# Performance work log

Hardware: AMD Instinct MI355X
Metric: run time of the kernel (lower is better)

The kernel has to match this reference:

```python
import jax, jax.numpy as jnp
import numpy as np

EPS = 1e-5


def gcn_conv(x, src, dst, n_nodes, W, b):
    # x: [B, N, Fin]; src/dst: [E+N] (self loops included); W: [Fout, Fin]
    h = jnp.einsum('bnf,of->bno', x, W)                      # [B, N, Fout]
    deg = jnp.zeros((n_nodes,), h.dtype).at[dst].add(1.0)    # in-degree of A+I
    dinv = jnp.where(deg > 0, 1.0 / jnp.sqrt(deg), 0.0)
    norm = dinv[src] * dinv[dst]                             # [E+N]
    msg = h[:, src, :] * norm[None, :, None]                 # gather along node axis
    out = jnp.zeros_like(h).at[:, dst, :].add(msg)           # scatter-add aggregate
    return out + b


def batchnorm_nodes(x, gamma, beta):
    # torch BatchNorm1d(N) on [B, N, C]: channel axis is N, stats over (B, C)
    mean = jnp.mean(x, axis=(0, 2), keepdims=True)
    var = jnp.mean(jnp.square(x - mean), axis=(0, 2), keepdims=True)
    xn = (x - mean) * jax.lax.rsqrt(var + EPS)
    return xn * gamma[None, :, None] + beta[None, :, None]


def setup_inputs() -> dict:
    key = jax.random.key(0)
    ks = jax.random.split(key, 20)
    B, N, FIN, D, OUT, E = 4096, 64, 67, 2048, 2, 512
    s = 0.1
    d = {}
    d['x_fingerprints'] = jax.random.normal(ks[0], (B, D), jnp.float32)
    d['x_node_features'] = jax.random.normal(ks[1], (B, N, FIN), jnp.float32)
    d['edge_list'] = jax.random.randint(ks[2], (2, E), 0, N)
    d['W1'] = jax.random.normal(ks[3], (64, FIN), jnp.float32) * s
    d['b1'] = jax.random.normal(ks[4], (64,), jnp.float32) * s
    d['g1'] = 1.0 + jax.random.normal(ks[5], (N,), jnp.float32) * s
    d['be1'] = jax.random.normal(ks[6], (N,), jnp.float32) * s
    d['W2'] = jax.random.normal(ks[7], (32, 64), jnp.float32) * s
    d['b2'] = jax.random.normal(ks[8], (32,), jnp.float32) * s
    d['g2'] = 1.0 + jax.random.normal(ks[9], (N,), jnp.float32) * s
    d['be2'] = jax.random.normal(ks[10], (N,), jnp.float32) * s
    d['Wl1'] = jax.random.normal(ks[11], (400, D), jnp.float32) * (s / 4)
    d['bl1'] = jax.random.normal(ks[12], (400,), jnp.float32) * s
    d['Wl2'] = jax.random.normal(ks[13], (64, 400), jnp.float32) * s
    d['bl2'] = jax.random.normal(ks[14], (64,), jnp.float32) * s
    d['Wfc'] = jax.random.normal(ks[15], (OUT, 96), jnp.float32) * s
    d['bfc'] = jax.random.normal(ks[16], (OUT,), jnp.float32) * s
    return d


def reference(x_fingerprints, x_node_features, edge_list, W1, b1, g1, be1,
              W2, b2, g2, be2, Wl1, bl1, Wl2, bl2, Wfc, bfc):
    B, N, _ = x_node_features.shape
    loops = jnp.arange(N)
    src = jnp.concatenate([edge_list[0], loops])  # add self loops (GCNConv default)
    dst = jnp.concatenate([edge_list[1], loops])
    g = gcn_conv(x_node_features, src, dst, N, W1, b1)
    g = jax.nn.relu(batchnorm_nodes(g, g1, be1))
    g = gcn_conv(g, src, dst, N, W2, b2)
    g = jax.nn.relu(batchnorm_nodes(g, g2, be2))           # [B, N, 32]
    pooled = jnp.max(g, axis=1)                             # global_max_pool -> [B, 32]
    h = jax.nn.relu(x_fingerprints @ Wl1.T + bl1)
    h = jax.nn.relu(h @ Wl2.T + bl2)                        # [B, 64]
    out = jnp.concatenate([pooled, h], axis=1) @ Wfc.T + bfc
    return out
```

## Files before the change

### kernel.cpp

```cpp
#include <hip/hip_runtime.h>
#include <hip/hip_bf16.h>
#include <math.h>

typedef __bf16 bf16;
typedef __attribute__((ext_vector_type(8))) __bf16 bf16x8;
typedef __attribute__((ext_vector_type(4))) __bf16 bf16x4;
typedef __attribute__((ext_vector_type(4))) float f32x4;

#define EPSBN 1e-5f
#define B_    4096
#define N_    64
#define FIN_  67
#define E_    512
#define TOT_E 576
#define NSLOT 128

__global__ __launch_bounds__(256) void k0_prep(const int* __restrict__ edge,
    float* __restrict__ partials,
    int* __restrict__ g_off, int* __restrict__ g_src, float* __restrict__ g_nrm)
{
    int tid = threadIdx.x;
    for (int i = blockIdx.x * 256 + tid; i < NSLOT * 64 * 4; i += gridDim.x * 256)
        partials[i] = 0.f;
    if (blockIdx.x != 0) return;

    __shared__ int ssrc[TOT_E], sdst[TOT_E];
    __shared__ int deg[N_], cnt[N_], off[N_ + 1];
    __shared__ float dinv[N_];
    for (int i = tid; i < TOT_E; i += 256) {
        int s, d;
        if (i < E_) { s = edge[i]; d = edge[E_ + i]; }
        else        { s = i - E_; d = i - E_; }
        ssrc[i] = s; sdst[i] = d;
    }
    if (tid < N_) { deg[tid] = 0; cnt[tid] = 0; }
    __syncthreads();
    for (int i = tid; i < TOT_E; i += 256) atomicAdd(&deg[sdst[i]], 1);
    __syncthreads();
    if (tid < N_) {
        dinv[tid] = rsqrtf((float)deg[tid]);
        int v = deg[tid];
        for (int o = 1; o < 64; o <<= 1) { int u = __shfl_up(v, o); if (tid >= o) v += u; }
        off[tid] = v - deg[tid];
        if (tid == 63) off[N_] = v;
    }
    __syncthreads();
    for (int i = tid; i < TOT_E; i += 256) {
        int d = sdst[i];
        int p = off[d] + atomicAdd(&cnt[d], 1);
        g_src[p] = ssrc[i];
        g_nrm[p] = dinv[ssrc[i]] * dinv[d];
    }
    if (tid <= N_) g_off[tid] = off[tid];
}

__global__ __launch_bounds__(256) void k1_gcn1(
    const float* __restrict__ x,
    const float* __restrict__ W1,
    const float* __restrict__ b1,
    const int* __restrict__ g_off, const int* __restrict__ g_src,
    const float* __restrict__ g_nrm,
    bf16* __restrict__ g1out,
    float* __restrict__ part1)
{
    __shared__ union {
        struct { bf16 xa[64 * 104]; bf16 wb[64 * 104]; } s0;
        struct { float hs[64 * 68]; } s1;
    } u;
    __shared__ int coff[N_ + 1];
    __shared__ int csrc[TOT_E];
    __shared__ float cnrm[TOT_E];

    int tid = threadIdx.x;
    int b = blockIdx.x;
    for (int i = tid; i <= N_; i += 256) coff[i] = g_off[i];
    for (int i = tid; i < TOT_E; i += 256) { csrc[i] = g_src[i]; cnrm[i] = g_nrm[i]; }

    const float* xb = x + (size_t)b * (N_ * FIN_);
    for (int i = tid; i < N_ * FIN_; i += 256) {
        int n = i / FIN_, f = i % FIN_;
        u.s0.xa[n * 104 + f] = (bf16)xb[i];
    }
    for (int i = tid; i < N_ * FIN_; i += 256) {
        int n = i / FIN_, f = i % FIN_;
        u.s0.wb[n * 104 + f] = (bf16)W1[i];
    }
    for (int i = tid; i < 64 * 29; i += 256) {
        int n = i / 29, f = 67 + i % 29;
        u.s0.xa[n * 104 + f] = (bf16)0.f;
        u.s0.wb[n * 104 + f] = (bf16)0.f;
    }
    __syncthreads();

    int w = tid >> 6, lane = tid & 63, q = lane >> 4, r15 = lane & 15;
    f32x4 z4 = {0.f, 0.f, 0.f, 0.f};
    f32x4 acc[4] = {z4, z4, z4, z4};
    int arow = w * 16 + r15;
#pragma unroll
    for (int kt = 0; kt < 3; ++kt) {
        bf16x8 a = *(const bf16x8*)&u.s0.xa[arow * 104 + kt * 32 + q * 8];
#pragma unroll
        for (int nt = 0; nt < 4; ++nt) {
            bf16x8 bb = *(const bf16x8*)&u.s0.wb[(nt * 16 + r15) * 104 + kt * 32 + q * 8];
            acc[nt] = __builtin_amdgcn_mfma_f32_16x16x32_bf16(a, bb, acc[nt], 0, 0, 0);
        }
    }
    __syncthreads();
#pragma unroll
    for (int nt = 0; nt < 4; ++nt)
#pragma unroll
        for (int r = 0; r < 4; ++r)
            u.s1.hs[(w * 16 + q * 4 + r) * 68 + nt * 16 + r15] = acc[nt][r];
    __syncthreads();

    int n = tid >> 2, oq = tid & 3;
    float a2[16];
#pragma unroll
    for (int j = 0; j < 16; ++j) a2[j] = 0.f;
    int e0 = coff[n], e1 = coff[n + 1];
    for (int e = e0; e < e1; ++e) {
        int s = csrc[e]; float wg = cnrm[e];
        const f32x4* hp = (const f32x4*)&u.s1.hs[s * 68 + oq * 16];
#pragma unroll
        for (int j4 = 0; j4 < 4; ++j4) {
            f32x4 hv = hp[j4];
            a2[j4 * 4 + 0] += wg * hv[0]; a2[j4 * 4 + 1] += wg * hv[1];
            a2[j4 * 4 + 2] += wg * hv[2]; a2[j4 * 4 + 3] += wg * hv[3];
        }
    }
    const f32x4* bp = (const f32x4*)&b1[oq * 16];
    float s1 = 0.f, s2 = 0.f;
    bf16x8 o0, o1;
#pragma unroll
    for (int j4 = 0; j4 < 4; ++j4) {
        f32x4 bv = bp[j4];
#pragma unroll
        for (int k = 0; k < 4; ++k) {
            float v = a2[j4 * 4 + k] + bv[k];
            s1 += v; s2 += v * v;
            if (j4 < 2) o0[j4 * 4 + k] = (bf16)v; else o1[(j4 - 2) * 4 + k] = (bf16)v;
        }
    }
    bf16* gp = g1out + ((size_t)b * 4096 + n * 64 + oq * 16);
    *(bf16x8*)gp = o0;
    *(bf16x8*)(gp + 8) = o1;
    s1 += __shfl_xor(s1, 1); s1 += __shfl_xor(s1, 2);
    s2 += __shfl_xor(s2, 1); s2 += __shfl_xor(s2, 2);
    if (oq == 0) {
        int slot = b & (NSLOT - 1);
        atomicAdd(&part1[(slot * 64 + n) * 2 + 0], s1);
        atomicAdd(&part1[(slot * 64 + n) * 2 + 1], s2);
    }
}

__global__ __launch_bounds__(64) void k_bnstats(
    const float* __restrict__ part,
    const float* __restrict__ gamma, const float* __restrict__ beta,
    float* __restrict__ scale, float* __restrict__ shift, float inv_count)
{
    int n = blockIdx.x, t = threadIdx.x;
    float s1 = part[(t * 64 + n) * 2] + part[((t + 64) * 64 + n) * 2];
    float s2 = part[(t * 64 + n) * 2 + 1] + part[((t + 64) * 64 + n) * 2 + 1];
#pragma unroll
    for (int o = 32; o > 0; o >>= 1) { s1 += __shfl_down(s1, o); s2 += __shfl_down(s2, o); }
    if (t == 0) {
        float mean = s1 * inv_count;
        float var = s2 * inv_count - mean * mean;
        float sc = gamma[n] * rsqrtf(var + EPSBN);
        scale[n] = sc;
        shift[n] = beta[n] - mean * sc;
    }
}

__global__ __launch_bounds__(256) void k3_gcn2(
    const bf16* __restrict__ g1out,
    const float* __restrict__ W2,
    const float* __restrict__ b2,
    const float* __restrict__ scale1, const float* __restrict__ shift1,
    const int* __restrict__ g_off, const int* __restrict__ g_src,
    const float* __restrict__ g_nrm,
    bf16* __restrict__ g2out,
    float* __restrict__ part2)
{
    __shared__ bf16 ya[64 * 72];
    __shared__ bf16 wb[32 * 72];
    __shared__ float hs[64 * 36];
    __shared__ int coff[N_ + 1];
    __shared__ int csrc[TOT_E];
    __shared__ float cnrm[TOT_E];
    __shared__ float ss1[64], sh1[64];

    int tid = threadIdx.x; int b = blockIdx.x;
    if (tid < 64) { ss1[tid] = scale1[tid]; sh1[tid] = shift1[tid]; }
    for (int i = tid; i <= N_; i += 256) coff[i] = g_off[i];
    for (int i = tid; i < TOT_E; i += 256) { csrc[i] = g_src[i]; cnrm[i] = g_nrm[i]; }
    for (int i = tid; i < 32 * 64; i += 256) {
        int o = i >> 6, f = i & 63;
        wb[o * 72 + f] = (bf16)W2[i];
    }
    __syncthreads();
    const bf16* gb = g1out + (size_t)b * 4096;
    for (int i = tid; i < 4096; i += 256) {
        int n = i >> 6;
        float v = (float)gb[i];
        float y = fmaxf(fmaf(ss1[n], v, sh1[n]), 0.f);
        ya[n * 72 + (i & 63)] = (bf16)y;
    }
    __syncthreads();

    int w = tid >> 6, lane = tid & 63, q = lane >> 4, r15 = lane & 15;
    f32x4 z4 = {0.f, 0.f, 0.f, 0.f};
    f32x4 acc[2] = {z4, z4};
#pragma unroll
    for (int kt = 0; kt < 2; ++kt) {
        bf16x8 a = *(const bf16x8*)&ya[(w * 16 + r15) * 72 + kt * 32 + q * 8];
#pragma unroll
        for (int nt = 0; nt < 2; ++nt) {
            bf16x8 bb = *(const bf16x8*)&wb[(nt * 16 + r15) * 72 + kt * 32 + q * 8];
            acc[nt] = __builtin_amdgcn_mfma_f32_16x16x32_bf16(a, bb, acc[nt], 0, 0, 0);
        }
    }
#pragma unroll
    for (int nt = 0; nt < 2; ++nt)
#pragma unroll
        for (int r = 0; r < 4; ++r)
            hs[(w * 16 + q * 4 + r) * 36 + nt * 16 + r15] = acc[nt][r];
    __syncthreads();

    int n = tid >> 2, oq = tid & 3;
    float a2[8] = {0, 0, 0, 0, 0, 0, 0, 0};
    int e0 = coff[n], e1 = coff[n + 1];
    for (int e = e0; e < e1; ++e) {
        int s = csrc[e]; float wg = cnrm[e];
        const f32x4* hp = (const f32x4*)&hs[s * 36 + oq * 8];
        f32x4 h0 = hp[0], h1v = hp[1];
        a2[0] += wg * h0[0]; a2[1] += wg * h0[1]; a2[2] += wg * h0[2]; a2[3] += wg * h0[3];
        a2[4] += wg * h1v[0]; a2[5] += wg * h1v[1]; a2[6] += wg * h1v[2]; a2[7] += wg * h1v[3];
    }
    const f32x4* bp = (const f32x4*)&b2[oq * 8];
    f32x4 b0 = bp[0], b1v = bp[1];
    float s1 = 0.f, s2 = 0.f; bf16x8 ov;
#pragma unroll
    for (int k = 0; k < 8; ++k) {
        float bias = (k < 4) ? b0[k] : b1v[k - 4];
        float v = a2[k] + bias;
        s1 += v; s2 += v * v;
        ov[k] = (bf16)v;
    }
    *(bf16x8*)(g2out + ((size_t)b * 2048 + n * 32 + oq * 8)) = ov;
    s1 += __shfl_xor(s1, 1); s1 += __shfl_xor(s1, 2);
    s2 += __shfl_xor(s2, 1); s2 += __shfl_xor(s2, 2);
    if (oq == 0) {
        int slot = b & (NSLOT - 1);
        atomicAdd(&part2[(slot * 64 + n) * 2 + 0], s1);
        atomicAdd(&part2[(slot * 64 + n) * 2 + 1], s2);
    }
}

__global__ __launch_bounds__(256) void k6_mlp1(
    const float* __restrict__ A,
    const float* __restrict__ Bw,
    float* __restrict__ part)
{
    __shared__ bf16 As[64 * 36];
    __shared__ bf16 Bs[64 * 36];
    int tid = threadIdx.x;
    int m0 = blockIdx.x * 64, n0 = blockIdx.y * 64, ks = blockIdx.z;
    int row = tid >> 2, seg = tid & 3;
    int w = tid >> 6, lane = tid & 63, q = lane >> 4, r15 = lane & 15;
    f32x4 z4 = {0.f, 0.f, 0.f, 0.f};
    f32x4 acc[4] = {z4, z4, z4, z4};
    const float* pA = A + (size_t)(m0 + row) * 2048 + ks * 512 + seg * 8;
    bool bvalid = (n0 + row) < 400;
    const float* pB = Bw + (size_t)(n0 + row) * 2048 + ks * 512 + seg * 8;

    f32x4 a0 = *(const f32x4*)pA;
    f32x4 a1 = *(const f32x4*)(pA + 4);
    f32x4 c0 = z4, c1 = z4;
    if (bvalid) { c0 = *(const f32x4*)pB; c1 = *(const f32x4*)(pB + 4); }

    for (int kt = 0; kt < 16; ++kt) {
        bf16x8 apk, bpk;
        apk[0] = (bf16)a0[0]; apk[1] = (bf16)a0[1]; apk[2] = (bf16)a0[2]; apk[3] = (bf16)a0[3];
        apk[4] = (bf16)a1[0]; apk[5] = (bf16)a1[1]; apk[6] = (bf16)a1[2]; apk[7] = (bf16)a1[3];
        bpk[0] = (bf16)c0[0]; bpk[1] = (bf16)c0[1]; bpk[2] = (bf16)c0[2]; bpk[3] = (bf16)c0[3];
        bpk[4] = (bf16)c1[0]; bpk[5] = (bf16)c1[1]; bpk[6] = (bf16)c1[2]; bpk[7] = (bf16)c1[3];
        __syncthreads();
        *(bf16x8*)&As[row * 36 + seg * 8] = apk;
        *(bf16x8*)&Bs[row * 36 + seg * 8] = bpk;
        __syncthreads();
        if (kt < 15) {
            pA += 32; pB += 32;
            a0 = *(const f32x4*)pA; a1 = *(const f32x4*)(pA + 4);
            if (bvalid) { c0 = *(const f32x4*)pB; c1 = *(const f32x4*)(pB + 4); }
        }
        bf16x8 a = *(const bf16x8*)&As[(w * 16 + r15) * 36 + q * 8];
#pragma unroll
        for (int nt = 0; nt < 4; ++nt) {
            bf16x8 bb = *(const bf16x8*)&Bs[(nt * 16 + r15) * 36 + q * 8];
            acc[nt] = __builtin_amdgcn_mfma_f32_16x16x32_bf16(a, bb, acc[nt], 0, 0, 0);
        }
    }
    float* pp = part + (size_t)ks * 1638400;
#pragma unroll
    for (int nt = 0; nt < 4; ++nt)
#pragma unroll
        for (int r = 0; r < 4; ++r) {
            int mm = m0 + w * 16 + q * 4 + r;
            int nn = n0 + nt * 16 + r15;
            if (nn < 400) pp[(size_t)mm * 400 + nn] = acc[nt][r];
        }
}

__global__ __launch_bounds__(256) void k6_reduce(
    const float* __restrict__ part,
    const float* __restrict__ bias,
    bf16* __restrict__ h1)
{
    int i = blockIdx.x * 256 + threadIdx.x;
    const f32x4* p = (const f32x4*)part;
    f32x4 s0 = p[i], s1v = p[i + 409600], s2v = p[i + 819200], s3v = p[i + 1228800];
    int nn = (i * 4) % 400;
    f32x4 bv = *(const f32x4*)&bias[nn];
    bf16x4 ov;
    ov[0] = (bf16)fmaxf(s0[0] + s1v[0] + s2v[0] + s3v[0] + bv[0], 0.f);
    ov[1] = (bf16)fmaxf(s0[1] + s1v[1] + s2v[1] + s3v[1] + bv[1], 0.f);
    ov[2] = (bf16)fmaxf(s0[2] + s1v[2] + s2v[2] + s3v[2] + bv[2], 0.f);
    ov[3] = (bf16)fmaxf(s0[3] + s1v[3] + s2v[3] + s3v[3] + bv[3], 0.f);
    *(bf16x4*)&h1[i * 4] = ov;
}

__global__ __launch_bounds__(256) void k7_mlp2(
    const bf16* __restrict__ A,
    const float* __restrict__ Bw,
    const float* __restrict__ bias,
    float* __restrict__ Cout)
{
    __shared__ bf16 As[16 * 416];
    int tid = threadIdx.x;
    int m0 = blockIdx.x * 16;
    for (int i = tid; i < 16 * 50; i += 256) {
        int rr = i / 50, cc = (i % 50) * 8;
        *(bf16x8*)&As[rr * 416 + cc] = *(const bf16x8*)(A + (size_t)(m0 + rr) * 400 + cc);
    }
    if (tid < 32) {
        int rr = tid >> 1, cc = 400 + (tid & 1) * 8;
        bf16x8 z;
#pragma unroll
        for (int k = 0; k < 8; ++k) z[k] = (bf16)0.f;
        *(bf16x8*)&As[rr * 416 + cc] = z;
    }
    __syncthreads();

    int w = tid >> 6, lane = tid & 63, q = lane >> 4, r15 = lane & 15;
    f32x4 acc = {0.f, 0.f, 0.f, 0.f};
    const float* pB = Bw + (size_t)(w * 16 + r15) * 400;
#pragma unroll 4
    for (int kt = 0; kt < 13; ++kt) {
        int k0 = kt * 32 + q * 8;
        bf16x8 a = *(const bf16x8*)&As[r15 * 416 + k0];
        bf16x8 bb;
#pragma unroll
        for (int k = 0; k < 8; ++k) bb[k] = (bf16)0.f;
        if (k0 < 400) {
            f32x4 c0 = *(const f32x4*)(pB + k0);
            f32x4 c1 = *(const f32x4*)(pB + k0 + 4);
            bb[0] = (bf16)c0[0]; bb[1] = (bf16)c0[1]; bb[2] = (bf16)c0[2]; bb[3] = (bf16)c0[3];
            bb[4] = (bf16)c1[0]; bb[5] = (bf16)c1[1]; bb[6] = (bf16)c1[2]; bb[7] = (bf16)c1[3];
        }
        acc = __builtin_amdgcn_mfma_f32_16x16x32_bf16(a, bb, acc, 0, 0, 0);
    }
#pragma unroll
    for (int r = 0; r < 4; ++r) {
        int mm = m0 + q * 4 + r;
        int nn = w * 16 + r15;
        float v = fmaxf(acc[r] + bias[nn], 0.f);
        Cout[(size_t)mm * 64 + nn] = v;
    }
}

__global__ __launch_bounds__(256) void k8_final(
    const bf16* __restrict__ g2out,
    const float* __restrict__ scale2, const float* __restrict__ shift2,
    const float* __restrict__ h2,
    const float* __restrict__ Wfc,
    const float* __restrict__ bfc,
    float* __restrict__ out)
{
    __shared__ float s2s[64], sh2s[64];
    int tid = threadIdx.x;
    if (tid < 64) { s2s[tid] = scale2[tid]; sh2s[tid] = shift2[tid]; }
    __syncthreads();
    int w = tid >> 6, lane = tid & 63;
    int b = blockIdx.x * 4 + w;
    int c = lane & 31, half = lane >> 5;
    const bf16* gb = g2out + (size_t)b * 2048;
    float mx = 0.f;
    for (int i = 0; i < 32; ++i) {
        int n = half * 32 + i;
        float v = (float)gb[n * 32 + c];
        float val = fmaf(s2s[n], v, sh2s[n]);
        mx = fmaxf(mx, val);
    }
    mx = fmaxf(mx, __shfl_xor(mx, 32));
    float h2v = h2[(size_t)b * 64 + lane];
#pragma unroll
    for (int o = 0; o < 2; ++o) {
        float t = h2v * Wfc[o * 96 + 32 + lane];
        if (half == 0) t += mx * Wfc[o * 96 + c];
#pragma unroll
        for (int off = 32; off > 0; off >>= 1) t += __shfl_xor(t, off);
        if (lane == 0) out[(size_t)b * 2 + o] = t + bfc[o];
    }
}

extern "C" void kernel_launch(void* const* d_in, const int* in_sizes, int n_in,
                              void* d_out, int out_size, void* d_ws, size_t ws_size,
                              hipStream_t stream)
{
    const float* x_fp   = (const float*)d_in[0];
    const float* x_node = (const float*)d_in[1];
    const int*   edge   = (const int*)d_in[2];
    const float* W1     = (const float*)d_in[3];
    const float* b1     = (const float*)d_in[4];
    const float* g1     = (const float*)d_in[5];
    const float* be1    = (const float*)d_in[6];
    const float* W2     = (const float*)d_in[7];
    const float* b2     = (const float*)d_in[8];
    const float* g2     = (const float*)d_in[9];
    const float* be2    = (const float*)d_in[10];
    const float* Wl1    = (const float*)d_in[11];
    const float* bl1    = (const float*)d_in[12];
    const float* Wl2    = (const float*)d_in[13];
    const float* bl2    = (const float*)d_in[14];
    const float* Wfc    = (const float*)d_in[15];
    const float* bfc    = (const float*)d_in[16];
    float* out = (float*)d_out;

    char* ws = (char*)d_ws;
    int*   csr_off = (int*)(ws);
    int*   csr_src = (int*)(ws + 512);
    float* csr_nrm = (float*)(ws + 3072);
    float* scale1  = (float*)(ws + 5632);
    float* shift1  = (float*)(ws + 5888);
    float* scale2  = (float*)(ws + 6144);
    float* shift2  = (float*)(ws + 6400);
    float* part1   = (float*)(ws + 8192);
    float* part2   = (float*)(ws + 8192 + 65536);
    bf16*  g1out   = (bf16*)(ws + 139264);
    float* part6   = (float*)(ws + 139264);
    bf16*  g2out   = (bf16*)(ws + 33693696ull);
    bf16*  h1      = (bf16*)(ws + 50470912ull);
    float* h2      = (float*)(ws + 53747712ull);

    k0_prep<<<dim3(64), dim3(256), 0, stream>>>(edge, part1, csr_off, csr_src, csr_nrm);
    k1_gcn1<<<dim3(4096), dim3(256), 0, stream>>>(x_node, W1, b1, csr_off, csr_src, csr_nrm,
                                                  g1out, part1);
    k_bnstats<<<dim3(64), dim3(64), 0, stream>>>(part1, g1, be1, scale1, shift1,
                                                 1.f / (4096.f * 64.f));
    k3_gcn2<<<dim3(4096), dim3(256), 0, stream>>>(g1out, W2, b2, scale1, shift1,
                                                  csr_off, csr_src, csr_nrm, g2out, part2);
    k_bnstats<<<dim3(64), dim3(64), 0, stream>>>(part2, g2, be2, scale2, shift2,
                                                 1.f / (4096.f * 32.f));
    k6_mlp1<<<dim3(64, 7, 4), dim3(256), 0, stream>>>(x_fp, Wl1, part6);
    k6_reduce<<<dim3(1600), dim3(256), 0, stream>>>(part6, bl1, h1);
    k7_mlp2<<<dim3(256), dim3(256), 0, stream>>>(h1, Wl2, bl2, h2);
    k8_final<<<dim3(1024), dim3(256), 0, stream>>>(g2out, scale2, shift2, h2, Wfc, bfc, out);
}
```

Baseline: 265.1 us.

## Replace CSR gather aggregation with dense normalized adjacency MFMA matmul

Builds a dense 64x64 normalized adjacency matrix once and performs GCN aggregation as a bf16 MFMA matmul instead of per-edge CSR gathers in shared memory. GCN kernels shrink to one wave per graph, holding weights, inputs and adjacency fragments in registers, with the transformed features transposed through a small LDS buffer. This removes the scalar edge-loop FMA work and the large LDS staging, but rounds the adjacency and intermediate features to bf16. It also reloads W and Ahat from global memory in every block and writes outputs with scattered 2-byte stores.

```diff
diff --git a/kernel.cpp b/kernel.cpp
--- a/kernel.cpp
+++ b/kernel.cpp
@@ -8,149 +8,161 @@
 typedef __attribute__((ext_vector_type(4))) float f32x4;
 
 #define EPSBN 1e-5f
-#define B_    4096
-#define N_    64
-#define FIN_  67
-#define E_    512
-#define TOT_E 576
 #define NSLOT 128
 
 __global__ __launch_bounds__(256) void k0_prep(const int* __restrict__ edge,
     float* __restrict__ partials,
-    int* __restrict__ g_off, int* __restrict__ g_src, float* __restrict__ g_nrm)
+    float* __restrict__ ahat)
 {
     int tid = threadIdx.x;
     for (int i = blockIdx.x * 256 + tid; i < NSLOT * 64 * 4; i += gridDim.x * 256)
         partials[i] = 0.f;
     if (blockIdx.x != 0) return;
 
-    __shared__ int ssrc[TOT_E], sdst[TOT_E];
-    __shared__ int deg[N_], cnt[N_], off[N_ + 1];
-    __shared__ float dinv[N_];
-    for (int i = tid; i < TOT_E; i += 256) {
-        int s, d;
-        if (i < E_) { s = edge[i]; d = edge[E_ + i]; }
-        else        { s = i - E_; d = i - E_; }
-        ssrc[i] = s; sdst[i] = d;
-    }
-    if (tid < N_) { deg[tid] = 0; cnt[tid] = 0; }
-    __syncthreads();
-    for (int i = tid; i < TOT_E; i += 256) atomicAdd(&deg[sdst[i]], 1);
-    __syncthreads();
-    if (tid < N_) {
-        dinv[tid] = rsqrtf((float)deg[tid]);
-        int v = deg[tid];
-        for (int o = 1; o < 64; o <<= 1) { int u = __shfl_up(v, o); if (tid >= o) v += u; }
-        off[tid] = v - deg[tid];
-        if (tid == 63) off[N_] = v;
-    }
-    __syncthreads();
-    for (int i = tid; i < TOT_E; i += 256) {
-        int d = sdst[i];
-        int p = off[d] + atomicAdd(&cnt[d], 1);
-        g_src[p] = ssrc[i];
-        g_nrm[p] = dinv[ssrc[i]] * dinv[d];
-    }
-    if (tid <= N_) g_off[tid] = off[tid];
-}
-
-__global__ __launch_bounds__(256) void k1_gcn1(
+    __shared__ float Ah[64 * 64];
+    __shared__ int deg[64];
+    __shared__ float dinv[64];
+    for (int i = tid; i < 4096; i += 256) Ah[i] = 0.f;
+    if (tid < 64) deg[tid] = 1;
+    __syncthreads();
+    for (int e = tid; e < 512; e += 256) atomicAdd(&deg[edge[512 + e]], 1);
+    __syncthreads();
+    if (tid < 64) dinv[tid] = rsqrtf((float)deg[tid]);
+    __syncthreads();
+    for (int e = tid; e < 512; e += 256) {
+        int s = edge[e], d = edge[512 + e];
+        atomicAdd(&Ah[d * 64 + s], dinv[s] * dinv[d]);
+    }
+    if (tid < 64) atomicAdd(&Ah[tid * 64 + tid], dinv[tid] * dinv[tid]);
+    __syncthreads();
+    for (int i = tid; i < 4096; i += 256) ahat[i] = Ah[i];
+}
+
+__global__ __launch_bounds__(64) void k1_gcn1(
     const float* __restrict__ x,
     const float* __restrict__ W1,
     const float* __restrict__ b1,
-    const int* __restrict__ g_off, const int* __restrict__ g_src,
-    const float* __restrict__ g_nrm,
+    const float* __restrict__ ahat,
     bf16* __restrict__ g1out,
     float* __restrict__ part1)
 {
-    __shared__ union {
-        struct { bf16 xa[64 * 104]; bf16 wb[64 * 104]; } s0;
-        struct { float hs[64 * 68]; } s1;
-    } u;
-    __shared__ int coff[N_ + 1];
-    __shared__ int csrc[TOT_E];
-    __shared__ float cnrm[TOT_E];
-
-    int tid = threadIdx.x;
+    __shared__ bf16 hT[64 * 72];
+    int lane = threadIdx.x;
+    int q = lane >> 4, r15 = lane & 15;
     int b = blockIdx.x;
-    for (int i = tid; i <= N_; i += 256) coff[i] = g_off[i];
-    for (int i = tid; i < TOT_E; i += 256) { csrc[i] = g_src[i]; cnrm[i] = g_nrm[i]; }
-
-    const float* xb = x + (size_t)b * (N_ * FIN_);
-    for (int i = tid; i < N_ * FIN_; i += 256) {
-        int n = i / FIN_, f = i % FIN_;
-        u.s0.xa[n * 104 + f] = (bf16)xb[i];
-    }
-    for (int i = tid; i < N_ * FIN_; i += 256) {
-        int n = i / FIN_, f = i % FIN_;
-        u.s0.wb[n * 104 + f] = (bf16)W1[i];
-    }
-    for (int i = tid; i < 64 * 29; i += 256) {
-        int n = i / 29, f = 67 + i % 29;
-        u.s0.xa[n * 104 + f] = (bf16)0.f;
-        u.s0.wb[n * 104 + f] = (bf16)0.f;
-    }
-    __syncthreads();
-
-    int w = tid >> 6, lane = tid & 63, q = lane >> 4, r15 = lane & 15;
+
+    bf16x8 aw[4][3];
+#pragma unroll
+    for (int mt = 0; mt < 4; ++mt) {
+        const float* wr = W1 + (mt * 16 + r15) * 67;
+#pragma unroll
+        for (int kt = 0; kt < 3; ++kt)
+#pragma unroll
+            for (int j = 0; j < 8; ++j) {
+                int f = kt * 32 + q * 8 + j;
+                float v = 0.f;
+                if (f < 67) v = wr[f];
+                aw[mt][kt][j] = (bf16)v;
+            }
+    }
+    const float* xb = x + (size_t)b * 4288;
+    bf16x8 xf[4][3];
+#pragma unroll
+    for (int nt = 0; nt < 4; ++nt) {
+        const float* xr = xb + (nt * 16 + r15) * 67;
+#pragma unroll
+        for (int kt = 0; kt < 3; ++kt)
+#pragma unroll
+            for (int j = 0; j < 8; ++j) {
+                int f = kt * 32 + q * 8 + j;
+                float v = 0.f;
+                if (f < 67) v = xr[f];
+                xf[nt][kt][j] = (bf16)v;
+            }
+    }
+
     f32x4 z4 = {0.f, 0.f, 0.f, 0.f};
-    f32x4 acc[4] = {z4, z4, z4, z4};
-    int arow = w * 16 + r15;
-#pragma unroll
-    for (int kt = 0; kt < 3; ++kt) {
-        bf16x8 a = *(const bf16x8*)&u.s0.xa[arow * 104 + kt * 32 + q * 8];
-#pragma unroll
-        for (int nt = 0; nt < 4; ++nt) {
-            bf16x8 bb = *(const bf16x8*)&u.s0.wb[(nt * 16 + r15) * 104 + kt * 32 + q * 8];
-            acc[nt] = __builtin_amdgcn_mfma_f32_16x16x32_bf16(a, bb, acc[nt], 0, 0, 0);
-        }
-    }
-    __syncthreads();
-#pragma unroll
-    for (int nt = 0; nt < 4; ++nt)
-#pragma unroll
-        for (int r = 0; r < 4; ++r)
-            u.s1.hs[(w * 16 + q * 4 + r) * 68 + nt * 16 + r15] = acc[nt][r];
-    __syncthreads();
-
-    int n = tid >> 2, oq = tid & 3;
-    float a2[16];
-#pragma unroll
-    for (int j = 0; j < 16; ++j) a2[j] = 0.f;
-    int e0 = coff[n], e1 = coff[n + 1];
-    for (int e = e0; e < e1; ++e) {
-        int s = csrc[e]; float wg = cnrm[e];
-        const f32x4* hp = (const f32x4*)&u.s1.hs[s * 68 + oq * 16];
-#pragma unroll
-        for (int j4 = 0; j4 < 4; ++j4) {
-            f32x4 hv = hp[j4];
-            a2[j4 * 4 + 0] += wg * hv[0]; a2[j4 * 4 + 1] += wg * hv[1];
-            a2[j4 * 4 + 2] += wg * hv[2]; a2[j4 * 4 + 3] += wg * hv[3];
-        }
-    }
-    const f32x4* bp = (const f32x4*)&b1[oq * 16];
-    float s1 = 0.f, s2 = 0.f;
-    bf16x8 o0, o1;
-#pragma unroll
-    for (int j4 = 0; j4 < 4; ++j4) {
-        f32x4 bv = bp[j4];
-#pragma unroll
-        for (int k = 0; k < 4; ++k) {
-            float v = a2[j4 * 4 + k] + bv[k];
-            s1 += v; s2 += v * v;
-            if (j4 < 2) o0[j4 * 4 + k] = (bf16)v; else o1[(j4 - 2) * 4 + k] = (bf16)v;
-        }
-    }
-    bf16* gp = g1out + ((size_t)b * 4096 + n * 64 + oq * 16);
-    *(bf16x8*)gp = o0;
-    *(bf16x8*)(gp + 8) = o1;
-    s1 += __shfl_xor(s1, 1); s1 += __shfl_xor(s1, 2);
-    s2 += __shfl_xor(s2, 1); s2 += __shfl_xor(s2, 2);
-    if (oq == 0) {
-        int slot = b & (NSLOT - 1);
-        atomicAdd(&part1[(slot * 64 + n) * 2 + 0], s1);
-        atomicAdd(&part1[(slot * 64 + n) * 2 + 1], s2);
-    }
+    f32x4 acc[4][4];
+#pragma unroll
+    for (int mt = 0; mt < 4; ++mt)
+#pragma unroll
+        for (int nt = 0; nt < 4; ++nt) acc[mt][nt] = z4;
+#pragma unroll
+    for (int kt = 0; kt < 3; ++kt)
+#pragma unroll
+        for (int mt = 0; mt < 4; ++mt)
+#pragma unroll
+            for (int nt = 0; nt < 4; ++nt)
+                acc[mt][nt] = __builtin_amdgcn_mfma_f32_16x16x32_bf16(aw[mt][kt], xf[nt][kt], acc[mt][nt], 0, 0, 0);
+
+#pragma unroll
+    for (int mt = 0; mt < 4; ++mt)
+#pragma unroll
+        for (int nt = 0; nt < 4; ++nt)
+#pragma unroll
+            for (int r = 0; r < 4; ++r)
+                hT[(mt * 16 + q * 4 + r) * 72 + nt * 16 + r15] = (bf16)acc[mt][nt][r];
+
+    bf16x8 ah[4][2];
+#pragma unroll
+    for (int mt = 0; mt < 4; ++mt)
+#pragma unroll
+        for (int kt = 0; kt < 2; ++kt) {
+            const float* ar = ahat + (mt * 16 + r15) * 64 + kt * 32 + q * 8;
+            f32x4 u = *(const f32x4*)ar;
+            f32x4 v = *(const f32x4*)(ar + 4);
+            ah[mt][kt][0] = (bf16)u[0]; ah[mt][kt][1] = (bf16)u[1];
+            ah[mt][kt][2] = (bf16)u[2]; ah[mt][kt][3] = (bf16)u[3];
+            ah[mt][kt][4] = (bf16)v[0]; ah[mt][kt][5] = (bf16)v[1];
+            ah[mt][kt][6] = (bf16)v[2]; ah[mt][kt][7] = (bf16)v[3];
+        }
+    __syncthreads();
+
+    bf16x8 hb[4][2];
+#pragma unroll
+    for (int ct = 0; ct < 4; ++ct)
+#pragma unroll
+        for (int kt = 0; kt < 2; ++kt)
+            hb[ct][kt] = *(const bf16x8*)&hT[(ct * 16 + r15) * 72 + kt * 32 + q * 8];
+
+    f32x4 o2[4][4];
+#pragma unroll
+    for (int mt = 0; mt < 4; ++mt)
+#pragma unroll
+        for (int ct = 0; ct < 4; ++ct) o2[mt][ct] = z4;
+#pragma unroll
+    for (int kt = 0; kt < 2; ++kt)
+#pragma unroll
+        for (int mt = 0; mt < 4; ++mt)
+#pragma unroll
+            for (int ct = 0; ct < 4; ++ct)
+                o2[mt][ct] = __builtin_amdgcn_mfma_f32_16x16x32_bf16(ah[mt][kt], hb[ct][kt], o2[mt][ct], 0, 0, 0);
+
+    float bv[4];
+#pragma unroll
+    for (int ct = 0; ct < 4; ++ct) bv[ct] = b1[ct * 16 + r15];
+
+    bf16* gp = g1out + (size_t)b * 4096;
+    int slot = b & (NSLOT - 1);
+#pragma unroll
+    for (int mt = 0; mt < 4; ++mt)
+#pragma unroll
+        for (int r = 0; r < 4; ++r) {
+            int n = mt * 16 + q * 4 + r;
+            float s1 = 0.f, s2 = 0.f;
+#pragma unroll
+            for (int ct = 0; ct < 4; ++ct) {
+                float v = o2[mt][ct][r] + bv[ct];
+                s1 += v; s2 += v * v;
+                gp[n * 64 + ct * 16 + r15] = (bf16)v;
+            }
+            s1 += __shfl_xor(s1, 1); s1 += __shfl_xor(s1, 2);
+            s2 += __shfl_xor(s2, 1); s2 += __shfl_xor(s2, 2);
+            if ((r15 & 3) == 0) {
+                atomicAdd(&part1[(slot * 64 + n) * 2 + 0], s1);
+                atomicAdd(&part1[(slot * 64 + n) * 2 + 1], s2);
+            }
+        }
 }
 
 __global__ __launch_bounds__(64) void k_bnstats(
@@ -172,89 +184,133 @@
     }
 }
 
-__global__ __launch_bounds__(256) void k3_gcn2(
+__global__ __launch_bounds__(64) void k3_gcn2(
     const bf16* __restrict__ g1out,
     const float* __restrict__ W2,
     const float* __restrict__ b2,
     const float* __restrict__ scale1, const float* __restrict__ shift1,
-    const int* __restrict__ g_off, const int* __restrict__ g_src,
-    const float* __restrict__ g_nrm,
+    const float* __restrict__ ahat,
     bf16* __restrict__ g2out,
     float* __restrict__ part2)
 {
-    __shared__ bf16 ya[64 * 72];
-    __shared__ bf16 wb[32 * 72];
-    __shared__ float hs[64 * 36];
-    __shared__ int coff[N_ + 1];
-    __shared__ int csrc[TOT_E];
-    __shared__ float cnrm[TOT_E];
-    __shared__ float ss1[64], sh1[64];
-
-    int tid = threadIdx.x; int b = blockIdx.x;
-    if (tid < 64) { ss1[tid] = scale1[tid]; sh1[tid] = shift1[tid]; }
-    for (int i = tid; i <= N_; i += 256) coff[i] = g_off[i];
-    for (int i = tid; i < TOT_E; i += 256) { csrc[i] = g_src[i]; cnrm[i] = g_nrm[i]; }
-    for (int i = tid; i < 32 * 64; i += 256) {
-        int o = i >> 6, f = i & 63;
-        wb[o * 72 + f] = (bf16)W2[i];
-    }
-    __syncthreads();
+    __shared__ bf16 hT[32 * 72];
+    int lane = threadIdx.x;
+    int q = lane >> 4, r15 = lane & 15;
+    int b = blockIdx.x;
+
+    bf16x8 aw[2][2];
+#pragma unroll
+    for (int mt = 0; mt < 2; ++mt)
+#pragma unroll
+        for (int kt = 0; kt < 2; ++kt) {
+            const float* wr = W2 + (mt * 16 + r15) * 64 + kt * 32 + q * 8;
+            f32x4 u = *(const f32x4*)wr;
+            f32x4 v = *(const f32x4*)(wr + 4);
+            aw[mt][kt][0] = (bf16)u[0]; aw[mt][kt][1] = (bf16)u[1];
+            aw[mt][kt][2] = (bf16)u[2]; aw[mt][kt][3] = (bf16)u[3];
+            aw[mt][kt][4] = (bf16)v[0]; aw[mt][kt][5] = (bf16)v[1];
+            aw[mt][kt][6] = (bf16)v[2]; aw[mt][kt][7] = (bf16)v[3];
+        }
+
     const bf16* gb = g1out + (size_t)b * 4096;
-    for (int i = tid; i < 4096; i += 256) {
-        int n = i >> 6;
-        float v = (float)gb[i];
-        float y = fmaxf(fmaf(ss1[n], v, sh1[n]), 0.f);
-        ya[n * 72 + (i & 63)] = (bf16)y;
-    }
-    __syncthreads();
-
-    int w = tid >> 6, lane = tid & 63, q = lane >> 4, r15 = lane & 15;
+    bf16x8 yf[4][2];
+#pragma unroll
+    for (int nt = 0; nt < 4; ++nt) {
+        int n = nt * 16 + r15;
+        float ss = scale1[n], sh = shift1[n];
+#pragma unroll
+        for (int kt = 0; kt < 2; ++kt) {
+            bf16x8 gv = *(const bf16x8*)(gb + n * 64 + kt * 32 + q * 8);
+#pragma unroll
+            for (int j = 0; j < 8; ++j) {
+                float v = fmaxf(fmaf(ss, (float)gv[j], sh), 0.f);
+                yf[nt][kt][j] = (bf16)v;
+            }
+        }
+    }
+
     f32x4 z4 = {0.f, 0.f, 0.f, 0.f};
-    f32x4 acc[2] = {z4, z4};
-#pragma unroll
-    for (int kt = 0; kt < 2; ++kt) {
-        bf16x8 a = *(const bf16x8*)&ya[(w * 16 + r15) * 72 + kt * 32 + q * 8];
-#pragma unroll
-        for (int nt = 0; nt < 2; ++nt) {
-            bf16x8 bb = *(const bf16x8*)&wb[(nt * 16 + r15) * 72 + kt * 32 + q * 8];
-            acc[nt] = __builtin_amdgcn_mfma_f32_16x16x32_bf16(a, bb, acc[nt], 0, 0, 0);
-        }
-    }
-#pragma unroll
-    for (int nt = 0; nt < 2; ++nt)
-#pragma unroll
-        for (int r = 0; r < 4; ++r)
-            hs[(w * 16 + q * 4 + r) * 36 + nt * 16 + r15] = acc[nt][r];
-    __syncthreads();
-
-    int n = tid >> 2, oq = tid & 3;
-    float a2[8] = {0, 0, 0, 0, 0, 0, 0, 0};
-    int e0 = coff[n], e1 = coff[n + 1];
-    for (int e = e0; e < e1; ++e) {
-        int s = csrc[e]; float wg = cnrm[e];
-        const f32x4* hp = (const f32x4*)&hs[s * 36 + oq * 8];
-        f32x4 h0 = hp[0], h1v = hp[1];
-        a2[0] += wg * h0[0]; a2[1] += wg * h0[1]; a2[2] += wg * h0[2]; a2[3] += wg * h0[3];
-        a2[4] += wg * h1v[0]; a2[5] += wg * h1v[1]; a2[6] += wg * h1v[2]; a2[7] += wg * h1v[3];
-    }
-    const f32x4* bp = (const f32x4*)&b2[oq * 8];
-    f32x4 b0 = bp[0], b1v = bp[1];
-    float s1 = 0.f, s2 = 0.f; bf16x8 ov;
-#pragma unroll
-    for (int k = 0; k < 8; ++k) {
-        float bias = (k < 4) ? b0[k] : b1v[k - 4];
-        float v = a2[k] + bias;
-        s1 += v; s2 += v * v;
-        ov[k] = (bf16)v;
-    }
-    *(bf16x8*)(g2out + ((size_t)b * 2048 + n * 32 + oq * 8)) = ov;
-    s1 += __shfl_xor(s1, 1); s1 += __shfl_xor(s1, 2);
-    s2 += __shfl_xor(s2, 1); s2 += __shfl_xor(s2, 2);
-    if (oq == 0) {
-        int slot = b & (NSLOT - 1);
-        atomicAdd(&part2[(slot * 64 + n) * 2 + 0], s1);
-        atomicAdd(&part2[(slot * 64 + n) * 2 + 1], s2);
-    }
+    f32x4 acc[2][4];
+#pragma unroll
+    for (int mt = 0; mt < 2; ++mt)
+#pragma unroll
+        for (int nt = 0; nt < 4; ++nt) acc[mt][nt] = z4;
+#pragma unroll
+    for (int kt = 0; kt < 2; ++kt)
+#pragma unroll
+        for (int mt = 0; mt < 2; ++mt)
+#pragma unroll
+            for (int nt = 0; nt < 4; ++nt)
+                acc[mt][nt] = __builtin_amdgcn_mfma_f32_16x16x32_bf16(aw[mt][kt], yf[nt][kt], acc[mt][nt], 0, 0, 0);
+
+#pragma unroll
+    for (int mt = 0; mt < 2; ++mt)
+#pragma unroll
+        for (int nt = 0; nt < 4; ++nt)
+#pragma unroll
+            for (int r = 0; r < 4; ++r)
+                hT[(mt * 16 + q * 4 + r) * 72 + nt * 16 + r15] = (bf16)acc[mt][nt][r];
+
+    bf16x8 ah[4][2];
+#pragma unroll
+    for (int mt = 0; mt < 4; ++mt)
+#pragma unroll
+        for (int kt = 0; kt < 2; ++kt) {
+            const float* ar = ahat + (mt * 16 + r15) * 64 + kt * 32 + q * 8;
+            f32x4 u = *(const f32x4*)ar;
+            f32x4 v = *(const f32x4*)(ar + 4);
+            ah[mt][kt][0] = (bf16)u[0]; ah[mt][kt][1] = (bf16)u[1];
+            ah[mt][kt][2] = (bf16)u[2]; ah[mt][kt][3] = (bf16)u[3];
+            ah[mt][kt][4] = (bf16)v[0]; ah[mt][kt][5] = (bf16)v[1];
+            ah[mt][kt][6] = (bf16)v[2]; ah[mt][kt][7] = (bf16)v[3];
+        }
+    __syncthreads();
+
+    bf16x8 hb[2][2];
+#pragma unroll
+    for (int ct = 0; ct < 2; ++ct)
+#pragma unroll
+        for (int kt = 0; kt < 2; ++kt)
+            hb[ct][kt] = *(const bf16x8*)&hT[(ct * 16 + r15) * 72 + kt * 32 + q * 8];
+
+    f32x4 o2[4][2];
+#pragma unroll
+    for (int mt = 0; mt < 4; ++mt)
+#pragma unroll
+        for (int ct = 0; ct < 2; ++ct) o2[mt][ct] = z4;
+#pragma unroll
+    for (int kt = 0; kt < 2; ++kt)
+#pragma unroll
+        for (int mt = 0; mt < 4; ++mt)
+#pragma unroll
+            for (int ct = 0; ct < 2; ++ct)
+                o2[mt][ct] = __builtin_amdgcn_mfma_f32_16x16x32_bf16(ah[mt][kt], hb[ct][kt], o2[mt][ct], 0, 0, 0);
+
+    float bv[2];
+#pragma unroll
+    for (int ct = 0; ct < 2; ++ct) bv[ct] = b2[ct * 16 + r15];
+
+    bf16* gp = g2out + (size_t)b * 2048;
+    int slot = b & (NSLOT - 1);
+#pragma unroll
+    for (int mt = 0; mt < 4; ++mt)
+#pragma unroll
+        for (int r = 0; r < 4; ++r) {
+            int n = mt * 16 + q * 4 + r;
+            float s1 = 0.f, s2 = 0.f;
+#pragma unroll
+            for (int ct = 0; ct < 2; ++ct) {
+                float v = o2[mt][ct][r] + bv[ct];
+                s1 += v; s2 += v * v;
+                gp[n * 32 + ct * 16 + r15] = (bf16)v;
+            }
+            s1 += __shfl_xor(s1, 1); s1 += __shfl_xor(s1, 2);
+            s2 += __shfl_xor(s2, 1); s2 += __shfl_xor(s2, 2);
+            if ((r15 & 3) == 0) {
+                atomicAdd(&part2[(slot * 64 + n) * 2 + 0], s1);
+                atomicAdd(&part2[(slot * 64 + n) * 2 + 1], s2);
+            }
+        }
 }
 
 __global__ __launch_bounds__(256) void k6_mlp1(
@@ -438,28 +494,25 @@
     float* out = (float*)d_out;
 
     char* ws = (char*)d_ws;
-    int*   csr_off = (int*)(ws);
-    int*   csr_src = (int*)(ws + 512);
-    float* csr_nrm = (float*)(ws + 3072);
-    float* scale1  = (float*)(ws + 5632);
-    float* shift1  = (float*)(ws + 5888);
-    float* scale2  = (float*)(ws + 6144);
-    float* shift2  = (float*)(ws + 6400);
-    float* part1   = (float*)(ws + 8192);
-    float* part2   = (float*)(ws + 8192 + 65536);
-    bf16*  g1out   = (bf16*)(ws + 139264);
-    float* part6   = (float*)(ws + 139264);
-    bf16*  g2out   = (bf16*)(ws + 33693696ull);
-    bf16*  h1      = (bf16*)(ws + 50470912ull);
-    float* h2      = (float*)(ws + 53747712ull);
-
-    k0_prep<<<dim3(64), dim3(256), 0, stream>>>(edge, part1, csr_off, csr_src, csr_nrm);
-    k1_gcn1<<<dim3(4096), dim3(256), 0, stream>>>(x_node, W1, b1, csr_off, csr_src, csr_nrm,
-                                                  g1out, part1);
+    float* ahat    = (float*)(ws);
+    float* scale1  = (float*)(ws + 16384);
+    float* shift1  = (float*)(ws + 16640);
+    float* scale2  = (float*)(ws + 16896);
+    float* shift2  = (float*)(ws + 17152);
+    float* part1   = (float*)(ws + 20480);
+    float* part2   = (float*)(ws + 86016);
+    bf16*  g1out   = (bf16*)(ws + 151552);
+    float* part6   = (float*)(ws + 151552);
+    bf16*  g2out   = (bf16*)(ws + 33705984ull);
+    bf16*  h1      = (bf16*)(ws + 50483200ull);
+    float* h2      = (float*)(ws + 53760000ull);
+
+    k0_prep<<<dim3(16), dim3(256), 0, stream>>>(edge, part1, ahat);
+    k1_gcn1<<<dim3(4096), dim3(64), 0, stream>>>(x_node, W1, b1, ahat, g1out, part1);
     k_bnstats<<<dim3(64), dim3(64), 0, stream>>>(part1, g1, be1, scale1, shift1,
                                                  1.f / (4096.f * 64.f));
-    k3_gcn2<<<dim3(4096), dim3(256), 0, stream>>>(g1out, W2, b2, scale1, shift1,
-                                                  csr_off, csr_src, csr_nrm, g2out, part2);
+    k3_gcn2<<<dim3(4096), dim3(64), 0, stream>>>(g1out, W2, b2, scale1, shift1, ahat,
+                                                 g2out, part2);
     k_bnstats<<<dim3(64), dim3(64), 0, stream>>>(part2, g2, be2, scale2, shift2,
                                                  1.f / (4096.f * 32.f));
     k6_mlp1<<<dim3(64, 7, 4), dim3(256), 0, stream>>>(x_fp, Wl1, part6);
```

Measured after the change: 453.7 us. 71.1% more time.
